# Performance work log

Measured on AMD Instinct MI355X. Metric: run time of the kernel, lower is better.

The kernel has to match this reference:

```python
import jax, jax.numpy as jnp
import numpy as np

ALPHA = 0.2  # LeakyReLU negative slope


def setup_inputs() -> dict:
    key = jax.random.key(0)
    k1, k2, k3, k4 = jax.random.split(key, 4)
    B, N, Fin, Fout = 8, 2048, 256, 256
    h = jax.random.normal(k1, (B, N, Fin), dtype=jnp.float32)
    # random 0/1 adjacency with guaranteed self-loops so every row has a neighbor
    adj = jax.random.randint(k2, (N, N), 0, 2).astype(jnp.float32)
    adj = jnp.maximum(adj, jnp.eye(N, dtype=jnp.float32))
    # xavier_uniform with gain=1.414
    def xavier(k, shape, gain=1.414):
        fan_in, fan_out = shape[0], shape[1]
        a = gain * np.sqrt(6.0 / (fan_in + fan_out))
        return jax.random.uniform(k, shape, dtype=jnp.float32, minval=-a, maxval=a)
    W = xavier(k3, (Fin, Fout))
    a = xavier(k4, (2 * Fout, 1))
    return {"h": h, "adj_matrix": adj, "W": W, "a": a}


def reference(h, adj_matrix, W, a):
    # h: [B, N, Fin], adj_matrix: [N, N], W: [Fin, Fout], a: [2*Fout, 1]
    Fout = W.shape[1]
    Wh = jnp.einsum("bnf,fo->bno", h, W)            # [B, N, Fout]
    a1, a2 = a[:Fout, 0], a[Fout:, 0]                 # split additive attention vector
    # e[b,i,j] = leakyrelu(Wh[b,i]@a1 + Wh[b,j]@a2) — equals concat([Wh_i,Wh_j])@a
    s1 = Wh @ a1                                      # [B, N]
    s2 = Wh @ a2                                      # [B, N]
    e = s1[:, :, None] + s2[:, None, :]               # [B, N, N]
    e = jnp.where(e >= 0, e, ALPHA * e)               # LeakyReLU
    e = jnp.where(adj_matrix[None] == 0, -jnp.inf, e)  # mask non-edges
    attention = jax.nn.softmax(e, axis=-1)            # [B, N, N]
    # dropout is identity in eval mode (training=False)
    h_prime = jnp.einsum("bij,bjo->bio", attention, Wh)
    return h_prime
```

## Files before the change

kernel.cpp:

```cpp
#include <hip/hip_runtime.h>
#include <cstdint>

#define BB 8
#define NN 2048
#define FF 256
#define LOG2E 1.4426950408889634f

typedef __attribute__((ext_vector_type(8))) short bf16x8;
typedef __attribute__((ext_vector_type(4))) float f32x4;

__device__ __forceinline__ unsigned short f2bf(float x){
  union { float f; unsigned u; } v; v.f = x;
  unsigned r = v.u + 0x7FFFu + ((v.u >> 16) & 1u);
  return (unsigned short)(r >> 16);
}
__device__ __forceinline__ unsigned pack2(float a, float b){
  return (unsigned)f2bf(a) | ((unsigned)f2bf(b) << 16);
}

__global__ __launch_bounds__(256) void k_wt(const float* __restrict__ W,
                                            unsigned short* __restrict__ Wt){
  int g = blockIdx.x * 256 + threadIdx.x;
  int o = g >> 8, k = g & 255;
  Wt[g] = f2bf(W[k * 256 + o]);
}

__global__ __launch_bounds__(256) void k_adjbits(const float* __restrict__ adj,
                                                 unsigned long long* __restrict__ ab){
  int i = blockIdx.x, tid = threadIdx.x;
  int w = tid >> 6, lane = tid & 63;
  #pragma unroll
  for (int seg = 0; seg < 8; seg++){
    int j = seg * 256 + tid;
    unsigned long long m = __ballot(adj[(size_t)i * NN + j] != 0.0f);
    if (lane == 0) ab[i * 32 + seg * 4 + w] = m;
  }
}

__global__ __launch_bounds__(256) void k_fused_gemm(const float* __restrict__ h,
                                                    const unsigned short* __restrict__ Wt,
                                                    const float* __restrict__ a,
                                                    unsigned short* __restrict__ WhT,
                                                    float* __restrict__ s1c,
                                                    float* __restrict__ s2c){
  __shared__ unsigned short As[64 * 72];
  __shared__ unsigned short Bs[256 * 72];
  __shared__ float s1p[4][64], s2p[4][64];
  const int tid = threadIdx.x;
  const int r0 = blockIdx.x * 64;
  const int b  = r0 >> 11;
  const int i0 = r0 & (NN - 1);
  const int w = tid >> 6, lane = tid & 63, lhi = lane >> 4, llo = lane & 15;
  const int wc = w * 64;

  f32x4 acc[4][4];
  #pragma unroll
  for (int i = 0; i < 4; i++)
    #pragma unroll
    for (int j = 0; j < 4; j++){ acc[i][j][0]=0.f; acc[i][j][1]=0.f; acc[i][j][2]=0.f; acc[i][j][3]=0.f; }

  const int ar = tid >> 2;
  const int as = (tid & 3) * 16;

  for (int k0 = 0; k0 < 256; k0 += 64){
    const float* hp = h + (size_t)(r0 + ar) * 256 + k0 + as;
    float4 v0 = *(const float4*)(hp);      float4 v1 = *(const float4*)(hp + 4);
    float4 v2 = *(const float4*)(hp + 8);  float4 v3 = *(const float4*)(hp + 12);
    uint4 q0 = make_uint4(pack2(v0.x, v0.y), pack2(v0.z, v0.w),
                          pack2(v1.x, v1.y), pack2(v1.z, v1.w));
    uint4 q1 = make_uint4(pack2(v2.x, v2.y), pack2(v2.z, v2.w),
                          pack2(v3.x, v3.y), pack2(v3.z, v3.w));
    *(uint4*)&As[ar * 72 + as]     = q0;
    *(uint4*)&As[ar * 72 + as + 8] = q1;
    #pragma unroll
    for (int p = 0; p < 8; p++){
      int o = p * 32 + (tid >> 3), col = (tid & 7) * 8;
      *(uint4*)&Bs[o * 72 + col] = *(const uint4*)(Wt + (size_t)o * 256 + k0 + col);
    }
    __syncthreads();
    #pragma unroll
    for (int kk = 0; kk < 2; kk++){
      bf16x8 af[4], bfr[4];
      #pragma unroll
      for (int t = 0; t < 4; t++)
        af[t] = *(const bf16x8*)&As[(t * 16 + llo) * 72 + kk * 32 + lhi * 8];
      #pragma unroll
      for (int t = 0; t < 4; t++)
        bfr[t] = *(const bf16x8*)&Bs[(wc + t * 16 + llo) * 72 + kk * 32 + lhi * 8];
      #pragma unroll
      for (int it = 0; it < 4; it++)
        #pragma unroll
        for (int ot = 0; ot < 4; ot++)
          acc[it][ot] = __builtin_amdgcn_mfma_f32_16x16x32_bf16(af[it], bfr[ot], acc[it][ot], 0, 0, 0);
    }
    __syncthreads();
  }

  float a1v[4], a2v[4];
  #pragma unroll
  for (int ot = 0; ot < 4; ot++){
    a1v[ot] = a[wc + ot * 16 + llo] * LOG2E;
    a2v[ot] = a[256 + wc + ot * 16 + llo] * LOG2E;
  }
  #pragma unroll
  for (int it = 0; it < 4; it++){
    #pragma unroll
    for (int q = 0; q < 4; q++){
      float p1 = 0.f, p2 = 0.f;
      #pragma unroll
      for (int ot = 0; ot < 4; ot++){
        p1 += acc[it][ot][q] * a1v[ot];
        p2 += acc[it][ot][q] * a2v[ot];
      }
      #pragma unroll
      for (int o = 1; o < 16; o <<= 1){ p1 += __shfl_xor(p1, o); p2 += __shfl_xor(p2, o); }
      if (llo == 0){
        s1p[w][it * 16 + lhi * 4 + q] = p1;
        s2p[w][it * 16 + lhi * 4 + q] = p2;
      }
    }
  }

  #pragma unroll
  for (int it = 0; it < 4; it++){
    #pragma unroll
    for (int ot = 0; ot < 4; ot++){
      int o = wc + ot * 16 + llo;
      uint2 u = make_uint2(pack2(acc[it][ot][0], acc[it][ot][1]),
                           pack2(acc[it][ot][2], acc[it][ot][3]));
      *(uint2*)&Bs[o * 72 + it * 16 + lhi * 4] = u;
    }
  }
  __syncthreads();

  if (tid < 64){
    s1c[r0 + tid] = s1p[0][tid] + s1p[1][tid] + s1p[2][tid] + s1p[3][tid];
    s2c[r0 + tid] = s2p[0][tid] + s2p[1][tid] + s2p[2][tid] + s2p[3][tid];
  }
  #pragma unroll
  for (int p = 0; p < 8; p++){
    int o = p * 32 + (tid >> 3), col = (tid & 7) * 8;
    *(uint4*)(WhT + (size_t)(b * 256 + o) * 2048 + i0 + col) = *(const uint4*)&Bs[o * 72 + col];
  }
}

__global__ __launch_bounds__(256) void k_attn(const float* __restrict__ s1c,
                                              const float* __restrict__ s2c,
                                              const unsigned short* __restrict__ WhT,
                                              const unsigned long long* __restrict__ ab,
                                              float* __restrict__ out){
  __shared__ float s2s[2048];
  __shared__ unsigned short Ps[64 * 72];
  __shared__ unsigned short Ws[256 * 72];
  __shared__ float s1s[64], lin[64], red[4];
  const int tid = threadIdx.x;
  const int b = blockIdx.y, i0 = blockIdx.x * 64;
  const int w = tid >> 6, lane = tid & 63, lhi = lane >> 4, llo = lane & 15;
  const int wc = w * 64;

  float vmax = -3.0e38f;
  #pragma unroll
  for (int k = 0; k < 2; k++){
    int idx = k * 256 + tid;
    float4 v = ((const float4*)(s2c + (size_t)b * NN))[idx];
    ((float4*)s2s)[idx] = v;
    vmax = fmaxf(vmax, fmaxf(fmaxf(v.x, v.y), fmaxf(v.z, v.w)));
  }
  #pragma unroll
  for (int o = 32; o; o >>= 1) vmax = fmaxf(vmax, __shfl_xor(vmax, o));
  if (lane == 0) red[w] = vmax;
  if (tid < 64) s1s[tid] = s1c[(size_t)b * NN + i0 + tid];
  __syncthreads();
  const float m2 = fmaxf(fmaxf(red[0], red[1]), fmaxf(red[2], red[3]));

  const int pi = tid >> 2;
  const int pj = (tid & 3) * 16;
  const float s1v = s1s[pi];
  const float xm = s1v + m2;
  const float mv = fmaxf(xm, 0.2f * xm);
  const unsigned long long* abrow = ab + (size_t)(i0 + pi) * 32;
  float rs = 0.f;

  f32x4 acc[4][4];
  #pragma unroll
  for (int i = 0; i < 4; i++)
    #pragma unroll
    for (int j = 0; j < 4; j++){ acc[i][j][0]=0.f; acc[i][j][1]=0.f; acc[i][j][2]=0.f; acc[i][j][3]=0.f; }

  for (int j0 = 0; j0 < NN; j0 += 64){
    #pragma unroll
    for (int p = 0; p < 8; p++){
      int o = p * 32 + (tid >> 3), col = (tid & 7) * 8;
      *(uint4*)&Ws[o * 72 + col] = *(const uint4*)(WhT + (size_t)(b * 256 + o) * 2048 + j0 + col);
    }
    unsigned bits = (unsigned)((abrow[j0 >> 6] >> pj) & 0xFFFFull);
    float pv[16];
    #pragma unroll
    for (int e = 0; e < 16; e++){
      float x = s1v + s2s[j0 + pj + e];
      float y = fmaxf(x, 0.2f * x) - mv;
      pv[e] = ((bits >> e) & 1u) ? __builtin_amdgcn_exp2f(y) : 0.0f;
      rs += pv[e];
    }
    uint4 q0 = make_uint4(pack2(pv[0], pv[1]),  pack2(pv[2], pv[3]),
                          pack2(pv[4], pv[5]),  pack2(pv[6], pv[7]));
    uint4 q1 = make_uint4(pack2(pv[8], pv[9]),  pack2(pv[10], pv[11]),
                          pack2(pv[12], pv[13]), pack2(pv[14], pv[15]));
    *(uint4*)&Ps[pi * 72 + pj]     = q0;
    *(uint4*)&Ps[pi * 72 + pj + 8] = q1;
    __syncthreads();
    #pragma unroll
    for (int kk = 0; kk < 2; kk++){
      bf16x8 af[4], bfr[4];
      #pragma unroll
      for (int t = 0; t < 4; t++)
        af[t] = *(const bf16x8*)&Ps[(t * 16 + llo) * 72 + kk * 32 + lhi * 8];
      #pragma unroll
      for (int t = 0; t < 4; t++)
        bfr[t] = *(const bf16x8*)&Ws[(wc + t * 16 + llo) * 72 + kk * 32 + lhi * 8];
      #pragma unroll
      for (int it = 0; it < 4; it++)
        #pragma unroll
        for (int ot = 0; ot < 4; ot++)
          acc[it][ot] = __builtin_amdgcn_mfma_f32_16x16x32_bf16(af[it], bfr[ot], acc[it][ot], 0, 0, 0);
    }
    __syncthreads();
  }

  rs += __shfl_xor(rs, 1);
  rs += __shfl_xor(rs, 2);
  if ((tid & 3) == 0) lin[pi] = 1.0f / rs;
  __syncthreads();

  #pragma unroll
  for (int it = 0; it < 4; it++){
    #pragma unroll
    for (int ot = 0; ot < 4; ot++){
      int col = wc + ot * 16 + llo;
      #pragma unroll
      for (int q = 0; q < 4; q++){
        int row = it * 16 + lhi * 4 + q;
        out[(size_t)(b * NN + i0 + row) * 256 + col] = acc[it][ot][q] * lin[row];
      }
    }
  }
}

extern "C" void kernel_launch(void* const* d_in, const int* in_sizes, int n_in,
                              void* d_out, int out_size, void* d_ws, size_t ws_size,
                              hipStream_t stream) {
  const float* h   = (const float*)d_in[0];
  const float* adj = (const float*)d_in[1];
  const float* W   = (const float*)d_in[2];
  const float* a   = (const float*)d_in[3];
  float* out = (float*)d_out;

  char* ws = (char*)d_ws;
  unsigned short* WhT      = (unsigned short*)(ws);
  unsigned short* Wt       = (unsigned short*)(ws + 8388608);
  unsigned long long* ab   = (unsigned long long*)(ws + 8519680);
  float* s1c               = (float*)(ws + 9043968);
  float* s2c               = (float*)(ws + 9109504);

  hipLaunchKernelGGL(k_wt,         dim3(256),    dim3(256), 0, stream, W, Wt);
  hipLaunchKernelGGL(k_adjbits,    dim3(2048),   dim3(256), 0, stream, adj, ab);
  hipLaunchKernelGGL(k_fused_gemm, dim3(256),    dim3(256), 0, stream, h, Wt, a, WhT, s1c, s2c);
  hipLaunchKernelGGL(k_attn,       dim3(32, 8),  dim3(256), 0, stream, s1c, s2c, WhT, ab, out);
}
```

Before: 143.3 us.

## Double-buffer B fragments in registers, use 512-thread blocks, merge prep kernels

The two GEMM-style kernels now load their B operand (Wt or WhT) straight from global memory into register fragments. The next tile's load is issued before the current tile's MFMAs, which replaces the LDS staging of the B tile. Blocks grow to 512 threads with eight waves, each covering 32 output columns. The adjacency-bit and weight-transpose prep kernels merge into one launch, and the bf16 pack for P switches to truncation via byte permute. This trades LDS traffic and one launch for more per-wave global loads, somewhat different rounding in P, and higher register pressure under launch_bounds(512,2).

```diff
diff --git a/kernel.cpp b/kernel.cpp
--- a/kernel.cpp
+++ b/kernel.cpp
@@ -1,9 +1,7 @@
 #include <hip/hip_runtime.h>
 #include <cstdint>
 
-#define BB 8
 #define NN 2048
-#define FF 256
 #define LOG2E 1.4426950408889634f
 
 typedef __attribute__((ext_vector_type(8))) short bf16x8;
@@ -17,88 +15,98 @@
 __device__ __forceinline__ unsigned pack2(float a, float b){
   return (unsigned)f2bf(a) | ((unsigned)f2bf(b) << 16);
 }
-
-__global__ __launch_bounds__(256) void k_wt(const float* __restrict__ W,
-                                            unsigned short* __restrict__ Wt){
-  int g = blockIdx.x * 256 + threadIdx.x;
-  int o = g >> 8, k = g & 255;
-  Wt[g] = f2bf(W[k * 256 + o]);
-}
-
-__global__ __launch_bounds__(256) void k_adjbits(const float* __restrict__ adj,
-                                                 unsigned long long* __restrict__ ab){
-  int i = blockIdx.x, tid = threadIdx.x;
-  int w = tid >> 6, lane = tid & 63;
-  #pragma unroll
-  for (int seg = 0; seg < 8; seg++){
-    int j = seg * 256 + tid;
-    unsigned long long m = __ballot(adj[(size_t)i * NN + j] != 0.0f);
-    if (lane == 0) ab[i * 32 + seg * 4 + w] = m;
-  }
-}
-
-__global__ __launch_bounds__(256) void k_fused_gemm(const float* __restrict__ h,
-                                                    const unsigned short* __restrict__ Wt,
-                                                    const float* __restrict__ a,
-                                                    unsigned short* __restrict__ WhT,
-                                                    float* __restrict__ s1c,
-                                                    float* __restrict__ s2c){
-  __shared__ unsigned short As[64 * 72];
-  __shared__ unsigned short Bs[256 * 72];
-  __shared__ float s1p[4][64], s2p[4][64];
+__device__ __forceinline__ unsigned permpack(unsigned hi, unsigned lo){
+  return __builtin_amdgcn_perm(hi, lo, 0x07060302u);
+}
+
+__global__ __launch_bounds__(256) void k_prep(const float* __restrict__ adj,
+                                              const float* __restrict__ W,
+                                              unsigned long long* __restrict__ ab,
+                                              unsigned short* __restrict__ Wt){
+  int tid = threadIdx.x;
+  if (blockIdx.x < 2048){
+    int i = blockIdx.x;
+    int w = tid >> 6, lane = tid & 63;
+    #pragma unroll
+    for (int seg = 0; seg < 8; seg++){
+      int j = seg * 256 + tid;
+      unsigned long long m = __ballot(adj[(size_t)i * NN + j] != 0.0f);
+      if (lane == 0) ab[i * 32 + seg * 4 + w] = m;
+    }
+  } else {
+    int g = (blockIdx.x - 2048) * 256 + tid;
+    int o = g >> 8, k = g & 255;
+    Wt[g] = f2bf(W[k * 256 + o]);
+  }
+}
+
+__global__ __launch_bounds__(512, 2) void k_fused_gemm(const float* __restrict__ h,
+                                                       const unsigned short* __restrict__ Wt,
+                                                       const float* __restrict__ a,
+                                                       unsigned short* __restrict__ WhT,
+                                                       float* __restrict__ s1c,
+                                                       float* __restrict__ s2c){
+  __shared__ __align__(16) unsigned short As[64 * 72];
+  __shared__ __align__(16) unsigned short Ts[256 * 72];
+  __shared__ float s1p[8][64], s2p[8][64];
   const int tid = threadIdx.x;
   const int r0 = blockIdx.x * 64;
   const int b  = r0 >> 11;
   const int i0 = r0 & (NN - 1);
   const int w = tid >> 6, lane = tid & 63, lhi = lane >> 4, llo = lane & 15;
-  const int wc = w * 64;
-
-  f32x4 acc[4][4];
+  const int wc = w * 32;
+
+  f32x4 acc[4][2];
   #pragma unroll
   for (int i = 0; i < 4; i++)
     #pragma unroll
-    for (int j = 0; j < 4; j++){ acc[i][j][0]=0.f; acc[i][j][1]=0.f; acc[i][j][2]=0.f; acc[i][j][3]=0.f; }
-
-  const int ar = tid >> 2;
-  const int as = (tid & 3) * 16;
-
-  for (int k0 = 0; k0 < 256; k0 += 64){
-    const float* hp = h + (size_t)(r0 + ar) * 256 + k0 + as;
-    float4 v0 = *(const float4*)(hp);      float4 v1 = *(const float4*)(hp + 4);
-    float4 v2 = *(const float4*)(hp + 8);  float4 v3 = *(const float4*)(hp + 12);
-    uint4 q0 = make_uint4(pack2(v0.x, v0.y), pack2(v0.z, v0.w),
-                          pack2(v1.x, v1.y), pack2(v1.z, v1.w));
-    uint4 q1 = make_uint4(pack2(v2.x, v2.y), pack2(v2.z, v2.w),
-                          pack2(v3.x, v3.y), pack2(v3.z, v3.w));
-    *(uint4*)&As[ar * 72 + as]     = q0;
-    *(uint4*)&As[ar * 72 + as + 8] = q1;
-    #pragma unroll
-    for (int p = 0; p < 8; p++){
-      int o = p * 32 + (tid >> 3), col = (tid & 7) * 8;
-      *(uint4*)&Bs[o * 72 + col] = *(const uint4*)(Wt + (size_t)o * 256 + k0 + col);
-    }
-    __syncthreads();
+    for (int j = 0; j < 2; j++){ acc[i][j][0]=0.f; acc[i][j][1]=0.f; acc[i][j][2]=0.f; acc[i][j][3]=0.f; }
+
+  const int ar = tid >> 3;
+  const int as_ = (tid & 7) * 8;
+
+  auto loadB = [&](int k0, bf16x8* dst){
+    #pragma unroll
+    for (int ot = 0; ot < 2; ot++)
+      #pragma unroll
+      for (int kk = 0; kk < 2; kk++)
+        dst[ot * 2 + kk] = *(const bf16x8*)(Wt + (size_t)(wc + ot * 16 + llo) * 256 + k0 + kk * 32 + lhi * 8);
+  };
+
+  auto stage = [&](int k0, bf16x8* cur, bf16x8* nxt, bool ld){
+    const float* hp = h + (size_t)(r0 + ar) * 256 + k0 + as_;
+    float4 v0 = *(const float4*)hp;
+    float4 v1 = *(const float4*)(hp + 4);
+    uint4 q = make_uint4(pack2(v0.x, v0.y), pack2(v0.z, v0.w),
+                         pack2(v1.x, v1.y), pack2(v1.z, v1.w));
+    __syncthreads();
+    *(uint4*)&As[ar * 72 + as_] = q;
+    __syncthreads();
+    if (ld) loadB(k0 + 64, nxt);
     #pragma unroll
     for (int kk = 0; kk < 2; kk++){
-      bf16x8 af[4], bfr[4];
-      #pragma unroll
-      for (int t = 0; t < 4; t++)
-        af[t] = *(const bf16x8*)&As[(t * 16 + llo) * 72 + kk * 32 + lhi * 8];
-      #pragma unroll
-      for (int t = 0; t < 4; t++)
-        bfr[t] = *(const bf16x8*)&Bs[(wc + t * 16 + llo) * 72 + kk * 32 + lhi * 8];
+      bf16x8 af[4];
+      #pragma unroll
+      for (int it = 0; it < 4; it++)
+        af[it] = *(const bf16x8*)&As[(it * 16 + llo) * 72 + kk * 32 + lhi * 8];
       #pragma unroll
       for (int it = 0; it < 4; it++)
         #pragma unroll
-        for (int ot = 0; ot < 4; ot++)
-          acc[it][ot] = __builtin_amdgcn_mfma_f32_16x16x32_bf16(af[it], bfr[ot], acc[it][ot], 0, 0, 0);
-    }
-    __syncthreads();
-  }
-
-  float a1v[4], a2v[4];
-  #pragma unroll
-  for (int ot = 0; ot < 4; ot++){
+        for (int ot = 0; ot < 2; ot++)
+          acc[it][ot] = __builtin_amdgcn_mfma_f32_16x16x32_bf16(af[it], cur[ot * 2 + kk], acc[it][ot], 0, 0, 0);
+    }
+  };
+
+  bf16x8 b0[4], b1[4];
+  loadB(0, b0);
+  stage(0,   b0, b1, true);
+  stage(64,  b1, b0, true);
+  stage(128, b0, b1, true);
+  stage(192, b1, b0, false);
+
+  float a1v[2], a2v[2];
+  #pragma unroll
+  for (int ot = 0; ot < 2; ot++){
     a1v[ot] = a[wc + ot * 16 + llo] * LOG2E;
     a2v[ot] = a[256 + wc + ot * 16 + llo] * LOG2E;
   }
@@ -106,12 +114,8 @@
   for (int it = 0; it < 4; it++){
     #pragma unroll
     for (int q = 0; q < 4; q++){
-      float p1 = 0.f, p2 = 0.f;
-      #pragma unroll
-      for (int ot = 0; ot < 4; ot++){
-        p1 += acc[it][ot][q] * a1v[ot];
-        p2 += acc[it][ot][q] * a2v[ot];
-      }
+      float p1 = acc[it][0][q] * a1v[0] + acc[it][1][q] * a1v[1];
+      float p2 = acc[it][0][q] * a2v[0] + acc[it][1][q] * a2v[1];
       #pragma unroll
       for (int o = 1; o < 16; o <<= 1){ p1 += __shfl_xor(p1, o); p2 += __shfl_xor(p2, o); }
       if (llo == 0){
@@ -124,118 +128,128 @@
   #pragma unroll
   for (int it = 0; it < 4; it++){
     #pragma unroll
-    for (int ot = 0; ot < 4; ot++){
+    for (int ot = 0; ot < 2; ot++){
       int o = wc + ot * 16 + llo;
       uint2 u = make_uint2(pack2(acc[it][ot][0], acc[it][ot][1]),
                            pack2(acc[it][ot][2], acc[it][ot][3]));
-      *(uint2*)&Bs[o * 72 + it * 16 + lhi * 4] = u;
+      *(uint2*)&Ts[o * 72 + it * 16 + lhi * 4] = u;
     }
   }
   __syncthreads();
 
   if (tid < 64){
-    s1c[r0 + tid] = s1p[0][tid] + s1p[1][tid] + s1p[2][tid] + s1p[3][tid];
-    s2c[r0 + tid] = s2p[0][tid] + s2p[1][tid] + s2p[2][tid] + s2p[3][tid];
-  }
-  #pragma unroll
-  for (int p = 0; p < 8; p++){
-    int o = p * 32 + (tid >> 3), col = (tid & 7) * 8;
-    *(uint4*)(WhT + (size_t)(b * 256 + o) * 2048 + i0 + col) = *(const uint4*)&Bs[o * 72 + col];
-  }
-}
-
-__global__ __launch_bounds__(256) void k_attn(const float* __restrict__ s1c,
-                                              const float* __restrict__ s2c,
-                                              const unsigned short* __restrict__ WhT,
-                                              const unsigned long long* __restrict__ ab,
-                                              float* __restrict__ out){
-  __shared__ float s2s[2048];
-  __shared__ unsigned short Ps[64 * 72];
-  __shared__ unsigned short Ws[256 * 72];
-  __shared__ float s1s[64], lin[64], red[4];
+    float t1 = 0.f, t2 = 0.f;
+    #pragma unroll
+    for (int g = 0; g < 8; g++){ t1 += s1p[g][tid]; t2 += s2p[g][tid]; }
+    s1c[r0 + tid] = t1;
+    s2c[r0 + tid] = t2;
+  }
+  #pragma unroll
+  for (int p = 0; p < 4; p++){
+    int o = p * 64 + (tid >> 3), col = (tid & 7) * 8;
+    *(uint4*)(WhT + (size_t)(b * 256 + o) * 2048 + i0 + col) = *(const uint4*)&Ts[o * 72 + col];
+  }
+}
+
+__global__ __launch_bounds__(512, 2) void k_attn(const float* __restrict__ s1c,
+                                                 const float* __restrict__ s2c,
+                                                 const unsigned short* __restrict__ WhT,
+                                                 const unsigned long long* __restrict__ ab,
+                                                 float* __restrict__ out){
+  __shared__ __align__(16) float s2s[2048];
+  __shared__ __align__(16) unsigned short Ps[64 * 72];
+  __shared__ float s1s[64], lin[64], red[8];
   const int tid = threadIdx.x;
   const int b = blockIdx.y, i0 = blockIdx.x * 64;
   const int w = tid >> 6, lane = tid & 63, lhi = lane >> 4, llo = lane & 15;
-  const int wc = w * 64;
-
-  float vmax = -3.0e38f;
-  #pragma unroll
-  for (int k = 0; k < 2; k++){
-    int idx = k * 256 + tid;
-    float4 v = ((const float4*)(s2c + (size_t)b * NN))[idx];
-    ((float4*)s2s)[idx] = v;
-    vmax = fmaxf(vmax, fmaxf(fmaxf(v.x, v.y), fmaxf(v.z, v.w)));
-  }
+  const int wc = w * 32;
+
+  float4 v = ((const float4*)(s2c + (size_t)b * NN))[tid];
+  ((float4*)s2s)[tid] = v;
+  float vmax = fmaxf(fmaxf(v.x, v.y), fmaxf(v.z, v.w));
   #pragma unroll
   for (int o = 32; o; o >>= 1) vmax = fmaxf(vmax, __shfl_xor(vmax, o));
   if (lane == 0) red[w] = vmax;
   if (tid < 64) s1s[tid] = s1c[(size_t)b * NN + i0 + tid];
   __syncthreads();
-  const float m2 = fmaxf(fmaxf(red[0], red[1]), fmaxf(red[2], red[3]));
-
-  const int pi = tid >> 2;
-  const int pj = (tid & 3) * 16;
+  float m2 = red[0];
+  #pragma unroll
+  for (int g = 1; g < 8; g++) m2 = fmaxf(m2, red[g]);
+
+  const int pi = tid >> 3;
+  const int pj = (tid & 7) * 8;
   const float s1v = s1s[pi];
   const float xm = s1v + m2;
   const float mv = fmaxf(xm, 0.2f * xm);
   const unsigned long long* abrow = ab + (size_t)(i0 + pi) * 32;
   float rs = 0.f;
 
-  f32x4 acc[4][4];
+  f32x4 acc[4][2];
   #pragma unroll
   for (int i = 0; i < 4; i++)
     #pragma unroll
-    for (int j = 0; j < 4; j++){ acc[i][j][0]=0.f; acc[i][j][1]=0.f; acc[i][j][2]=0.f; acc[i][j][3]=0.f; }
-
-  for (int j0 = 0; j0 < NN; j0 += 64){
-    #pragma unroll
-    for (int p = 0; p < 8; p++){
-      int o = p * 32 + (tid >> 3), col = (tid & 7) * 8;
-      *(uint4*)&Ws[o * 72 + col] = *(const uint4*)(WhT + (size_t)(b * 256 + o) * 2048 + j0 + col);
-    }
-    unsigned bits = (unsigned)((abrow[j0 >> 6] >> pj) & 0xFFFFull);
-    float pv[16];
-    #pragma unroll
-    for (int e = 0; e < 16; e++){
-      float x = s1v + s2s[j0 + pj + e];
+    for (int j = 0; j < 2; j++){ acc[i][j][0]=0.f; acc[i][j][1]=0.f; acc[i][j][2]=0.f; acc[i][j][3]=0.f; }
+
+  auto loadB = [&](int j0, bf16x8* dst){
+    #pragma unroll
+    for (int ot = 0; ot < 2; ot++)
+      #pragma unroll
+      for (int kk = 0; kk < 2; kk++)
+        dst[ot * 2 + kk] = *(const bf16x8*)(WhT + (size_t)(b * 256 + wc + ot * 16 + llo) * 2048 + j0 + kk * 32 + lhi * 8);
+  };
+
+  auto stage = [&](int jj, bf16x8* cur, bf16x8* nxt, bool ld){
+    unsigned bits = (unsigned)((abrow[jj >> 6] >> pj) & 0xFFull);
+    float4 xa = *(const float4*)&s2s[jj + pj];
+    float4 xb = *(const float4*)&s2s[jj + pj + 4];
+    float xs[8] = {xa.x, xa.y, xa.z, xa.w, xb.x, xb.y, xb.z, xb.w};
+    unsigned pu[8];
+    #pragma unroll
+    for (int e = 0; e < 8; e++){
+      float x = s1v + xs[e];
       float y = fmaxf(x, 0.2f * x) - mv;
-      pv[e] = ((bits >> e) & 1u) ? __builtin_amdgcn_exp2f(y) : 0.0f;
-      rs += pv[e];
-    }
-    uint4 q0 = make_uint4(pack2(pv[0], pv[1]),  pack2(pv[2], pv[3]),
-                          pack2(pv[4], pv[5]),  pack2(pv[6], pv[7]));
-    uint4 q1 = make_uint4(pack2(pv[8], pv[9]),  pack2(pv[10], pv[11]),
-                          pack2(pv[12], pv[13]), pack2(pv[14], pv[15]));
-    *(uint4*)&Ps[pi * 72 + pj]     = q0;
-    *(uint4*)&Ps[pi * 72 + pj + 8] = q1;
-    __syncthreads();
+      float p = ((bits >> e) & 1u) ? __builtin_amdgcn_exp2f(y) : 0.0f;
+      unsigned u = __float_as_uint(p) & 0xFFFF0000u;
+      rs += __uint_as_float(u);
+      pu[e] = u;
+    }
+    uint4 q = make_uint4(permpack(pu[1], pu[0]), permpack(pu[3], pu[2]),
+                         permpack(pu[5], pu[4]), permpack(pu[7], pu[6]));
+    __syncthreads();
+    *(uint4*)&Ps[pi * 72 + pj] = q;
+    __syncthreads();
+    if (ld) loadB(jj + 64, nxt);
     #pragma unroll
     for (int kk = 0; kk < 2; kk++){
-      bf16x8 af[4], bfr[4];
-      #pragma unroll
-      for (int t = 0; t < 4; t++)
-        af[t] = *(const bf16x8*)&Ps[(t * 16 + llo) * 72 + kk * 32 + lhi * 8];
-      #pragma unroll
-      for (int t = 0; t < 4; t++)
-        bfr[t] = *(const bf16x8*)&Ws[(wc + t * 16 + llo) * 72 + kk * 32 + lhi * 8];
+      bf16x8 af[4];
+      #pragma unroll
+      for (int it = 0; it < 4; it++)
+        af[it] = *(const bf16x8*)&Ps[(it * 16 + llo) * 72 + kk * 32 + lhi * 8];
       #pragma unroll
       for (int it = 0; it < 4; it++)
         #pragma unroll
-        for (int ot = 0; ot < 4; ot++)
-          acc[it][ot] = __builtin_amdgcn_mfma_f32_16x16x32_bf16(af[it], bfr[ot], acc[it][ot], 0, 0, 0);
-    }
-    __syncthreads();
+        for (int ot = 0; ot < 2; ot++)
+          acc[it][ot] = __builtin_amdgcn_mfma_f32_16x16x32_bf16(af[it], cur[ot * 2 + kk], acc[it][ot], 0, 0, 0);
+    }
+  };
+
+  bf16x8 b0[4], b1[4];
+  loadB(0, b0);
+  for (int j0 = 0; j0 < NN; j0 += 128){
+    stage(j0,      b0, b1, true);
+    stage(j0 + 64, b1, b0, (j0 + 128) < NN);
   }
 
   rs += __shfl_xor(rs, 1);
   rs += __shfl_xor(rs, 2);
-  if ((tid & 3) == 0) lin[pi] = 1.0f / rs;
+  rs += __shfl_xor(rs, 4);
+  if ((tid & 7) == 0) lin[pi] = 1.0f / rs;
   __syncthreads();
 
   #pragma unroll
   for (int it = 0; it < 4; it++){
     #pragma unroll
-    for (int ot = 0; ot < 4; ot++){
+    for (int ot = 0; ot < 2; ot++){
       int col = wc + ot * 16 + llo;
       #pragma unroll
       for (int q = 0; q < 4; q++){
@@ -262,8 +276,7 @@
   float* s1c               = (float*)(ws + 9043968);
   float* s2c               = (float*)(ws + 9109504);
 
-  hipLaunchKernelGGL(k_wt,         dim3(256),    dim3(256), 0, stream, W, Wt);
-  hipLaunchKernelGGL(k_adjbits,    dim3(2048),   dim3(256), 0, stream, adj, ab);
-  hipLaunchKernelGGL(k_fused_gemm, dim3(256),    dim3(256), 0, stream, h, Wt, a, WhT, s1c, s2c);
-  hipLaunchKernelGGL(k_attn,       dim3(32, 8),  dim3(256), 0, stream, s1c, s2c, WhT, ab, out);
-}
+  hipLaunchKernelGGL(k_prep,       dim3(2304),   dim3(256), 0, stream, adj, W, ab, Wt);
+  hipLaunchKernelGGL(k_fused_gemm, dim3(256),    dim3(512), 0, stream, h, Wt, a, WhT, s1c, s2c);
+  hipLaunchKernelGGL(k_attn,       dim3(32, 8),  dim3(512), 0, stream, s1c, s2c, WhT, ab, out);
+}
```

Result: faster. 139.1 us (-2.9%).
